# Kernel optimization log

Measured on AMD Instinct MI355X. Metric: run time of the kernel, lower is better.

## Reference

```python
import jax, jax.numpy as jnp
import numpy as np

N = 50000   # nodes
E = 800000  # edges
H = 128     # hidden dim
V = 50000   # feats_per_node (embedding vocab)


def setup_inputs() -> dict:
    key = jax.random.key(0)
    ks = jax.random.split(key, 16)
    s = 0.05  # keep activations in a sane range
    return {
        "node_ids": jax.random.randint(ks[0], (N,), 0, V),
        "src": jax.random.randint(ks[1], (E,), 0, N),
        "dst": jnp.sort(jax.random.randint(ks[2], (E,), 0, N)),
        "emb": jax.random.normal(ks[3], (V, H), jnp.float32) * s,
        "W_pool1": jax.random.normal(ks[4], (H, H), jnp.float32) * s,
        "b_pool1": jax.random.normal(ks[5], (H,), jnp.float32) * s,
        "W_self1": jax.random.normal(ks[6], (H, H), jnp.float32) * s,
        "W_neigh1": jax.random.normal(ks[7], (H, H), jnp.float32) * s,
        "b1": jax.random.normal(ks[8], (H,), jnp.float32) * s,
        "W_pool2": jax.random.normal(ks[9], (H, H), jnp.float32) * s,
        "b_pool2": jax.random.normal(ks[10], (H,), jnp.float32) * s,
        "W_self2": jax.random.normal(ks[11], (H, H), jnp.float32) * s,
        "W_neigh2": jax.random.normal(ks[12], (H, H), jnp.float32) * s,
        "b2": jax.random.normal(ks[13], (H,), jnp.float32) * s,
    }


def _sage_pool_layer(h, src, dst, W_pool, b_pool, W_self, W_neigh, b):
    # DGL SAGEConv('pool'): per-src MLP, gather over edges, segmented max per dst.
    m = jax.nn.relu(h @ W_pool + b_pool)              # [N, H]
    msgs = m[src]                                     # [E, H] gather
    agg = jax.ops.segment_max(msgs, dst, num_segments=N,
                              indices_are_sorted=True)  # [N, H]
    agg = jnp.where(jnp.isneginf(agg), 0.0, agg)      # zero-in-degree -> 0 (DGL semantics)
    return h @ W_self + agg @ W_neigh + b


def reference(node_ids, src, dst, emb,
              W_pool1, b_pool1, W_self1, W_neigh1, b1,
              W_pool2, b_pool2, W_self2, W_neigh2, b2):
    h = emb[node_ids]                                 # embedding_h on 1-hot indices
    h = _sage_pool_layer(h, src, dst, W_pool1, b_pool1, W_self1, W_neigh1, b1)
    h = _sage_pool_layer(h, src, dst, W_pool2, b_pool2, W_self2, W_neigh2, b2)
    return h
```

## Files before the change

### kernel.cpp

```cpp
#include <hip/hip_runtime.h>

#define HD 128

typedef __attribute__((ext_vector_type(8))) short short8;
typedef __attribute__((ext_vector_type(4))) float floatx4;
typedef __attribute__((ext_vector_type(2))) unsigned short ushort2v;
typedef __attribute__((ext_vector_type(4))) unsigned int uint4v;

typedef unsigned short ushort_t;
typedef unsigned int uint_t;

__device__ __forceinline__ ushort_t f2b(float f) {
    union { float f; uint_t u; } v; v.f = f;
    uint_t r = v.u + 0x7fff + ((v.u >> 16) & 1);
    return (ushort_t)(r >> 16);
}
__device__ __forceinline__ short8 cvt8(const float* __restrict__ p) {
    float4 u = *(const float4*)p, v = *(const float4*)(p + 4);
    short8 r;
    r[0] = (short)f2b(u.x); r[1] = (short)f2b(u.y); r[2] = (short)f2b(u.z); r[3] = (short)f2b(u.w);
    r[4] = (short)f2b(v.x); r[5] = (short)f2b(v.y); r[6] = (short)f2b(v.z); r[7] = (short)f2b(v.w);
    return r;
}
__device__ __forceinline__ uint_t pkmax(uint_t a, uint_t b) {
    return __builtin_bit_cast(uint_t,
        __builtin_elementwise_max(__builtin_bit_cast(ushort2v, a),
                                  __builtin_bit_cast(ushort2v, b)));
}
__device__ __forceinline__ int lbound(const int* __restrict__ dst, int E, int v) {
    int lo = 0, hi = E;
    while (lo < hi) {
        int mid = (lo + hi) >> 1;
        if (dst[mid] < v) lo = mid + 1; else hi = mid;
    }
    return lo;
}

__global__ __launch_bounds__(256) void k_prep(const int* __restrict__ dst, int E,
                                              int* __restrict__ rp, int N,
                                              int* __restrict__ srcPad,
                                              ushort_t* __restrict__ bufM,
                                              const float* W0, const float* W1,
                                              const float* W2, const float* W3,
                                              const float* W4, const float* W5,
                                              ushort_t* __restrict__ Wpk,
                                              int nbR, int nbP) {
    int b = blockIdx.x;
    if (b < nbR) {
        int i = b * 256 + threadIdx.x;
        if (i > N) return;
        rp[i] = lbound(dst, E, i);
    } else if (b < nbR + nbP) {
        int bb = b - nbR;
        const float* Ws[6] = {W0, W1, W2, W3, W4, W5};
        int mat = bb >> 6;
        int o = ((bb & 63) << 8) + threadIdx.x;
        int j = o & 7, l = (o >> 3) & 63, s = (o >> 9) & 3, t = o >> 11;
        int k = s * 32 + ((l >> 4) & 3) * 8 + j;
        int n = t * 16 + (l & 15);
        Wpk[(size_t)mat * 16384 + o] = f2b(Ws[mat][k * HD + n]);
    } else {
        int bb = b - nbR - nbP;
        if (bb == 0 && threadIdx.x < 64) {
            uint_t* mz = (uint_t*)bufM;
            mz[(size_t)(threadIdx.x >> 4) * ((size_t)(N + 1) * 16)
               + (size_t)N * 16 + (threadIdx.x & 15)] = 0u;
        }
        int idx = bb * 256 + threadIdx.x;
        if (idx < N * 32) srcPad[idx] = N;
    }
}

__device__ __forceinline__ void stage_w(const ushort_t* __restrict__ g,
                                        ushort_t* l, int tid) {
#pragma unroll
    for (int i = 0; i < 8; ++i) {
        int off = i * 2048 + tid * 8;
        *(short8*)&l[off] = *(const short8*)&g[off];
    }
}
__device__ __forceinline__ void stage_w_half(const ushort_t* __restrict__ g,
                                             ushort_t* l, int tid) {
#pragma unroll
    for (int i = 0; i < 4; ++i) {
        int off = i * 2048 + tid * 8;
        *(short8*)&l[off] = *(const short8*)&g[off];
    }
}

__device__ __forceinline__ void store_bf16(ushort_t* __restrict__ m, int row,
                                           int colbase, const floatx4& acc,
                                           const float4& bv, bool relu, int N) {
    if (row >= N) return;
    float v0 = acc[0] + bv.x, v1 = acc[1] + bv.y, v2 = acc[2] + bv.z, v3 = acc[3] + bv.w;
    if (relu) { v0 = fmaxf(v0, 0.f); v1 = fmaxf(v1, 0.f); v2 = fmaxf(v2, 0.f); v3 = fmaxf(v3, 0.f); }
    uint2 o; o.x = (uint_t)f2b(v0) | ((uint_t)f2b(v1) << 16);
    o.y = (uint_t)f2b(v2) | ((uint_t)f2b(v3) << 16);
    *(uint2*)&m[(size_t)row * HD + colbase] = o;
}

__device__ __forceinline__ void store_m(ushort_t* __restrict__ m, int row,
                                        int colbase, const floatx4& acc,
                                        const float4& bv, int N) {
    if (row >= N) return;
    float v0 = fmaxf(acc[0] + bv.x, 0.f), v1 = fmaxf(acc[1] + bv.y, 0.f);
    float v2 = fmaxf(acc[2] + bv.z, 0.f), v3 = fmaxf(acc[3] + bv.w, 0.f);
    uint2 o; o.x = (uint_t)f2b(v0) | ((uint_t)f2b(v1) << 16);
    o.y = (uint_t)f2b(v2) | ((uint_t)f2b(v3) << 16);
    size_t addr = (size_t)(colbase >> 5) * ((size_t)(N + 1) * 32)
                + (size_t)row * 32 + (colbase & 31);
    *(uint2*)&m[addr] = o;
}

__global__ __launch_bounds__(256) void k_gather_pool(const int* __restrict__ ids,
                                                     const float* __restrict__ emb,
                                                     const ushort_t* __restrict__ Wpk,
                                                     const float* __restrict__ bias,
                                                     ushort_t* __restrict__ h0,
                                                     ushort_t* __restrict__ m, int N,
                                                     const int* __restrict__ src,
                                                     const int* __restrict__ dst,
                                                     const int* __restrict__ rp,
                                                     int* __restrict__ srcPad,
                                                     int E, int nb_gemm) {
    if ((int)blockIdx.x >= nb_gemm) {
        int e = (blockIdx.x - nb_gemm) * 256 + threadIdx.x;
        if (e < E) {
            int node = dst[e];
            int j = e - rp[node];
            if (j < 32) srcPad[(size_t)node * 32 + j] = src[e];
        }
        return;
    }
    __shared__ ushort_t Wl[16384];
    int wave = blockIdx.x * 4 + (threadIdx.x >> 6);
    int row0 = wave * 32;
    int l = threadIdx.x & 63;
    int ar0 = row0 + (l & 15); if (ar0 >= N) ar0 = N - 1;
    int ar1 = ar0 + 16;        if (ar1 >= N) ar1 = N - 1;
    int ac = (l >> 4) * 8;
    int id0 = ids[ar0], id1 = ids[ar1];
    short8 a0[4], a1[4];
#pragma unroll
    for (int s = 0; s < 4; ++s) {
        a0[s] = cvt8(&emb[(size_t)id0 * HD + s * 32 + ac]);
        a1[s] = cvt8(&emb[(size_t)id1 * HD + s * 32 + ac]);
    }
    stage_w(Wpk, Wl, threadIdx.x);
    __syncthreads();
    if (row0 >= N) return;
#pragma unroll
    for (int s = 0; s < 4; ++s) {
        *(short8*)&h0[(size_t)ar0 * HD + s * 32 + ac] = a0[s];
        *(short8*)&h0[(size_t)ar1 * HD + s * 32 + ac] = a1[s];
    }
    int g0 = row0 + (l & 15), g1 = g0 + 16;
    int cb0 = ((l >> 4) & 3) * 4;
#pragma unroll
    for (int t = 0; t < 8; ++t) {
        floatx4 acc0 = {0.f, 0.f, 0.f, 0.f};
        floatx4 acc1 = {0.f, 0.f, 0.f, 0.f};
#pragma unroll
        for (int s = 0; s < 4; ++s) {
            short8 w = *(const short8*)&Wl[(t * 4 + s) * 512 + l * 8];
            acc0 = __builtin_amdgcn_mfma_f32_16x16x32_bf16(w, a0[s], acc0, 0, 0, 0);
            acc1 = __builtin_amdgcn_mfma_f32_16x16x32_bf16(w, a1[s], acc1, 0, 0, 0);
        }
        int cb = t * 16 + cb0;
        float4 bv = *(const float4*)&bias[cb];
        store_m(m, g0, cb, acc0, bv, N);
        store_m(m, g1, cb, acc1, bv, N);
    }
}

__global__ __launch_bounds__(256) void k_pool(const ushort_t* __restrict__ h,
                                              const ushort_t* __restrict__ Wpk,
                                              const float* __restrict__ bias,
                                              ushort_t* __restrict__ m, int N) {
    __shared__ ushort_t Wl[8192];
    int colhalf = blockIdx.x & 1;
    int wave = (blockIdx.x >> 1) * 4 + (threadIdx.x >> 6);
    int row0 = wave * 32;
    int l = threadIdx.x & 63;
    int ar0 = row0 + (l & 15); if (ar0 >= N) ar0 = N - 1;
    int ar1 = ar0 + 16;        if (ar1 >= N) ar1 = N - 1;
    int ac = (l >> 4) * 8;
    short8 a0[4], a1[4];
#pragma unroll
    for (int s = 0; s < 4; ++s) {
        a0[s] = *(const short8*)&h[(size_t)ar0 * HD + s * 32 + ac];
        a1[s] = *(const short8*)&h[(size_t)ar1 * HD + s * 32 + ac];
    }
    stage_w_half(Wpk + colhalf * 8192, Wl, threadIdx.x);
    __syncthreads();
    if (row0 >= N) return;
    int g0 = row0 + (l & 15), g1 = g0 + 16;
    int cb0 = ((l >> 4) & 3) * 4;
#pragma unroll
    for (int t = 0; t < 4; ++t) {
        floatx4 acc0 = {0.f, 0.f, 0.f, 0.f};
        floatx4 acc1 = {0.f, 0.f, 0.f, 0.f};
#pragma unroll
        for (int s = 0; s < 4; ++s) {
            short8 w = *(const short8*)&Wl[(t * 4 + s) * 512 + l * 8];
            acc0 = __builtin_amdgcn_mfma_f32_16x16x32_bf16(w, a0[s], acc0, 0, 0, 0);
            acc1 = __builtin_amdgcn_mfma_f32_16x16x32_bf16(w, a1[s], acc1, 0, 0, 0);
        }
        int cb = (colhalf * 4 + t) * 16 + cb0;
        float4 bv = *(const float4*)&bias[cb];
        store_m(m, g0, cb, acc0, bv, N);
        store_m(m, g1, cb, acc1, bv, N);
    }
}

__global__ __launch_bounds__(256) void k_segmax(const ushort_t* __restrict__ m,
                                                const int* __restrict__ srcPad,
                                                const int* __restrict__ src,
                                                const int* __restrict__ rp,
                                                ushort_t* __restrict__ agg, int N) {
    int cg = blockIdx.x & 3;
    int l = threadIdx.x & 63;
    int slot = l >> 2;
    int c = l & 3;
    int node0 = ((blockIdx.x >> 2) * 4 + (threadIdx.x >> 6)) * 4;
    if (node0 >= N) return;
    const uint_t* __restrict__ mg = (const uint_t*)m + (size_t)cg * ((size_t)(N + 1) * 16);
    uint_t* __restrict__ aggw = (uint_t*)agg;

    int nd[4], s0[4], s1[4], bg[4], en[4];
#pragma unroll
    for (int nn = 0; nn < 4; ++nn) {
        int node = node0 + nn; if (node >= N) node = N - 1;
        nd[nn] = node;
    }
#pragma unroll
    for (int nn = 0; nn < 4; ++nn) {
        s0[nn] = srcPad[(size_t)nd[nn] * 32 + slot];
        s1[nn] = srcPad[(size_t)nd[nn] * 32 + 16 + slot];
    }
#pragma unroll
    for (int nn = 0; nn < 4; ++nn) {
        bg[nn] = rp[nd[nn]];
        en[nn] = rp[nd[nn] + 1];
    }
    uint4v p0[4], p1[4];
#pragma unroll
    for (int nn = 0; nn < 4; ++nn) {
        p0[nn] = *(const uint4v*)&mg[(size_t)s0[nn] * 16 + c * 4];
        p1[nn] = *(const uint4v*)&mg[(size_t)s1[nn] * 16 + c * 4];
    }
    int b0 = slot & 1, b1 = (slot >> 1) & 1;
#pragma unroll
    for (int nn = 0; nn < 4; ++nn) {
        int node = node0 + nn;
        uint_t a0 = pkmax(p0[nn].x, p1[nn].x);
        uint_t a1 = pkmax(p0[nn].y, p1[nn].y);
        uint_t a2 = pkmax(p0[nn].z, p1[nn].z);
        uint_t a3 = pkmax(p0[nn].w, p1[nn].w);
        int deg = en[nn] - bg[nn];
        if (__builtin_expect(deg > 32, 0)) {
            int dm1 = deg - 1;
            for (int o = 32; o < deg; o += 16) {
                int i = o + slot; if (i > dm1) i = dm1;
                int s = src[bg[nn] + i];
                uint4v p = *(const uint4v*)&mg[(size_t)s * 16 + c * 4];
                a0 = pkmax(a0, p.x); a1 = pkmax(a1, p.y);
                a2 = pkmax(a2, p.z); a3 = pkmax(a3, p.w);
            }
        }
        uint_t q0 = b0 ? a2 : a0, q1 = b0 ? a3 : a1;
        uint_t r0 = b0 ? a0 : a2, r1 = b0 ? a1 : a3;
        q0 = pkmax(q0, (uint_t)__shfl_xor((int)r0, 4));
        q1 = pkmax(q1, (uint_t)__shfl_xor((int)r1, 4));
        uint_t s_ = b1 ? q1 : q0, t_ = b1 ? q0 : q1;
        s_ = pkmax(s_, (uint_t)__shfl_xor((int)t_, 8));
        s_ = pkmax(s_, (uint_t)__shfl_xor((int)s_, 16));
        s_ = pkmax(s_, (uint_t)__shfl_xor((int)s_, 32));
        if (slot < 4 && node < N)
            __builtin_nontemporal_store(s_,
                &aggw[(size_t)node * 64 + cg * 16 + c * 4 + 2 * b0 + b1]);
    }
}

template <bool F32OUT>
__global__ __launch_bounds__(256) void k_dual(const ushort_t* __restrict__ h,
                                              const ushort_t* __restrict__ agg,
                                              const ushort_t* __restrict__ WsPk,
                                              const ushort_t* __restrict__ WnPk,
                                              const float* __restrict__ bias,
                                              void* __restrict__ outp, int N) {
    __shared__ ushort_t Wl[16384];
    int colhalf = blockIdx.x & 1;
    int wave = (blockIdx.x >> 1) * 4 + (threadIdx.x >> 6);
    int row0 = wave * 32;
    int l = threadIdx.x & 63;
    int ar0 = row0 + (l & 15); if (ar0 >= N) ar0 = N - 1;
    int ar1 = ar0 + 16;        if (ar1 >= N) ar1 = N - 1;
    int ac = (l >> 4) * 8;
    short8 ah0[4], ah1[4], ag0[4], ag1[4];
#pragma unroll
    for (int s = 0; s < 4; ++s) {
        ah0[s] = *(const short8*)&h[(size_t)ar0 * HD + s * 32 + ac];
        ah1[s] = *(const short8*)&h[(size_t)ar1 * HD + s * 32 + ac];
        ag0[s] = *(const short8*)&agg[(size_t)ar0 * HD + s * 32 + ac];
        ag1[s] = *(const short8*)&agg[(size_t)ar1 * HD + s * 32 + ac];
    }
    stage_w_half(WsPk + colhalf * 8192, Wl, threadIdx.x);
    stage_w_half(WnPk + colhalf * 8192, Wl + 8192, threadIdx.x);
    __syncthreads();
    if (row0 >= N) return;
    int g0 = row0 + (l & 15), g1 = g0 + 16;
    int cb0 = ((l >> 4) & 3) * 4;
#pragma unroll
    for (int t = 0; t < 4; ++t) {
        floatx4 acc0 = {0.f, 0.f, 0.f, 0.f};
        floatx4 acc1 = {0.f, 0.f, 0.f, 0.f};
#pragma unroll
        for (int s = 0; s < 4; ++s) {
            short8 ws = *(const short8*)&Wl[(t * 4 + s) * 512 + l * 8];
            acc0 = __builtin_amdgcn_mfma_f32_16x16x32_bf16(ws, ah0[s], acc0, 0, 0, 0);
            acc1 = __builtin_amdgcn_mfma_f32_16x16x32_bf16(ws, ah1[s], acc1, 0, 0, 0);
        }
#pragma unroll
        for (int s = 0; s < 4; ++s) {
            short8 wn = *(const short8*)&Wl[8192 + (t * 4 + s) * 512 + l * 8];
            acc0 = __builtin_amdgcn_mfma_f32_16x16x32_bf16(wn, ag0[s], acc0, 0, 0, 0);
            acc1 = __builtin_amdgcn_mfma_f32_16x16x32_bf16(wn, ag1[s], acc1, 0, 0, 0);
        }
        int cb = (colhalf * 4 + t) * 16 + cb0;
        float4 bv = *(const float4*)&bias[cb];
        if (F32OUT) {
            float* out = (float*)outp;
            if (g0 < N) {
                float4 v = make_float4(acc0[0] + bv.x, acc0[1] + bv.y,
                                       acc0[2] + bv.z, acc0[3] + bv.w);
                *(float4*)&out[(size_t)g0 * HD + cb] = v;
            }
            if (g1 < N) {
                float4 v = make_float4(acc1[0] + bv.x, acc1[1] + bv.y,
                                       acc1[2] + bv.z, acc1[3] + bv.w);
                *(float4*)&out[(size_t)g1 * HD + cb] = v;
            }
        } else {
            ushort_t* out = (ushort_t*)outp;
            store_bf16(out, g0, cb, acc0, bv, false, N);
            store_bf16(out, g1, cb, acc1, bv, false, N);
        }
    }
}

extern "C" void kernel_launch(void* const* d_in, const int* in_sizes, int n_in,
                              void* d_out, int out_size, void* d_ws, size_t ws_size,
                              hipStream_t stream) {
    const int*   node_ids = (const int*)d_in[0];
    const int*   src      = (const int*)d_in[1];
    const int*   dst      = (const int*)d_in[2];
    const float* emb      = (const float*)d_in[3];
    const float* Wp1      = (const float*)d_in[4];
    const float* bp1      = (const float*)d_in[5];
    const float* Ws1      = (const float*)d_in[6];
    const float* Wn1      = (const float*)d_in[7];
    const float* b1       = (const float*)d_in[8];
    const float* Wp2      = (const float*)d_in[9];
    const float* bp2      = (const float*)d_in[10];
    const float* Ws2      = (const float*)d_in[11];
    const float* Wn2      = (const float*)d_in[12];
    const float* b2       = (const float*)d_in[13];
    float* out = (float*)d_out;

    const int N = in_sizes[0];
    const int E = in_sizes[1];

    char* ws = (char*)d_ws;
    int* rp = (int*)ws;
    size_t off = (((size_t)(N + 1) * 4) + 255) & ~(size_t)255;
    int* srcPad = (int*)(ws + off);
    off += (((size_t)N * 32 * 4) + 255) & ~(size_t)255;
    ushort_t* Wpk  = (ushort_t*)(ws + off);
    ushort_t* h0   = Wpk + 6 * 16384;
    ushort_t* h1   = h0 + (size_t)N * HD;
    ushort_t* bufM = h1 + (size_t)N * HD;
    ushort_t* bufA = bufM + (size_t)(N + 1) * HD;

    const int nbR = (N + 1 + 255) / 256;
    const int nbP = 6 * 64;
    const int nbI = ((N * 32) + 255) / 256;
    const int nbE = (E + 255) / 256;
    const int nb_gemm = (N + 127) / 128;
    const int nb_half = nb_gemm * 2;
    const int nb_seg  = ((N + 15) / 16) * 4;

    k_prep<<<nbR + nbP + nbI, 256, 0, stream>>>(dst, E, rp, N, srcPad, bufM,
                                                Wp1, Ws1, Wn1, Wp2, Ws2, Wn2,
                                                Wpk, nbR, nbP);

    const ushort_t* Wp1k = Wpk;
    const ushort_t* Ws1k = Wpk + 16384;
    const ushort_t* Wn1k = Wpk + 2 * 16384;
    const ushort_t* Wp2k = Wpk + 3 * 16384;
    const ushort_t* Ws2k = Wpk + 4 * 16384;
    const ushort_t* Wn2k = Wpk + 5 * 16384;

    k_gather_pool<<<nb_gemm + nbE, 256, 0, stream>>>(node_ids, emb, Wp1k, bp1,
                                                     h0, bufM, N,
                                                     src, dst, rp, srcPad, E, nb_gemm);
    k_segmax<<<nb_seg, 256, 0, stream>>>(bufM, srcPad, src, rp, bufA, N);
    k_dual<false><<<nb_half, 256, 0, stream>>>(h0, bufA, Ws1k, Wn1k, b1, h1, N);
    k_pool<<<nb_half, 256, 0, stream>>>(h1, Wp2k, bp2, bufM, N);
    k_segmax<<<nb_seg, 256, 0, stream>>>(bufM, srcPad, src, rp, bufA, N);
    k_dual<true><<<nb_half, 256, 0, stream>>>(h1, bufA, Ws2k, Wn2k, b2, out, N);
}
```

Before: 228.3 us.

## Fuse layer-1 self/neighbor GEMM with layer-2 pool GEMM in one kernel

Replaces the separate k_dual<false> and k_pool launches with a single k_dual_pool kernel. Each block computes the full 128-column h1 tile for 128 rows, writes it to global memory and also to a swizzled LDS tile, then reuses it from LDS as the A operand for the layer-2 pool GEMM. This removes one kernel launch and the global re-read of h1, and changes the grid from split column halves to full-width rows. In exchange LDS use doubles to 64KB per block, more weight staging and syncs happen per block, and the grid has half as many blocks, which may lower occupancy.

New measurement: 219.0 us. -4.1%, faster.

```diff
diff --git a/kernel.cpp b/kernel.cpp
--- a/kernel.cpp
+++ b/kernel.cpp
@@ -173,46 +173,6 @@
     }
 }
 
-__global__ __launch_bounds__(256) void k_pool(const ushort_t* __restrict__ h,
-                                              const ushort_t* __restrict__ Wpk,
-                                              const float* __restrict__ bias,
-                                              ushort_t* __restrict__ m, int N) {
-    __shared__ ushort_t Wl[8192];
-    int colhalf = blockIdx.x & 1;
-    int wave = (blockIdx.x >> 1) * 4 + (threadIdx.x >> 6);
-    int row0 = wave * 32;
-    int l = threadIdx.x & 63;
-    int ar0 = row0 + (l & 15); if (ar0 >= N) ar0 = N - 1;
-    int ar1 = ar0 + 16;        if (ar1 >= N) ar1 = N - 1;
-    int ac = (l >> 4) * 8;
-    short8 a0[4], a1[4];
-#pragma unroll
-    for (int s = 0; s < 4; ++s) {
-        a0[s] = *(const short8*)&h[(size_t)ar0 * HD + s * 32 + ac];
-        a1[s] = *(const short8*)&h[(size_t)ar1 * HD + s * 32 + ac];
-    }
-    stage_w_half(Wpk + colhalf * 8192, Wl, threadIdx.x);
-    __syncthreads();
-    if (row0 >= N) return;
-    int g0 = row0 + (l & 15), g1 = g0 + 16;
-    int cb0 = ((l >> 4) & 3) * 4;
-#pragma unroll
-    for (int t = 0; t < 4; ++t) {
-        floatx4 acc0 = {0.f, 0.f, 0.f, 0.f};
-        floatx4 acc1 = {0.f, 0.f, 0.f, 0.f};
-#pragma unroll
-        for (int s = 0; s < 4; ++s) {
-            short8 w = *(const short8*)&Wl[(t * 4 + s) * 512 + l * 8];
-            acc0 = __builtin_amdgcn_mfma_f32_16x16x32_bf16(w, a0[s], acc0, 0, 0, 0);
-            acc1 = __builtin_amdgcn_mfma_f32_16x16x32_bf16(w, a1[s], acc1, 0, 0, 0);
-        }
-        int cb = (colhalf * 4 + t) * 16 + cb0;
-        float4 bv = *(const float4*)&bias[cb];
-        store_m(m, g0, cb, acc0, bv, N);
-        store_m(m, g1, cb, acc1, bv, N);
-    }
-}
-
 __global__ __launch_bounds__(256) void k_segmax(const ushort_t* __restrict__ m,
                                                 const int* __restrict__ srcPad,
                                                 const int* __restrict__ src,
@@ -279,6 +239,104 @@
         if (slot < 4 && node < N)
             __builtin_nontemporal_store(s_,
                 &aggw[(size_t)node * 64 + cg * 16 + c * 4 + 2 * b0 + b1]);
+    }
+}
+
+__global__ __launch_bounds__(256) void k_dual_pool(const ushort_t* __restrict__ h,
+                                                   const ushort_t* __restrict__ agg,
+                                                   const ushort_t* __restrict__ WsPk,
+                                                   const ushort_t* __restrict__ WnPk,
+                                                   const ushort_t* __restrict__ WpPk,
+                                                   const float* __restrict__ bias1,
+                                                   const float* __restrict__ biasP,
+                                                   ushort_t* __restrict__ h1out,
+                                                   ushort_t* __restrict__ m2, int N) {
+    __shared__ ushort_t Wl[16384];
+    __shared__ ushort_t Ht[16384];
+    int wave = threadIdx.x >> 6;
+    int row0 = blockIdx.x * 128 + wave * 32;
+    int l = threadIdx.x & 63;
+    int ar0 = row0 + (l & 15); if (ar0 >= N) ar0 = N - 1;
+    int ar1 = ar0 + 16;        if (ar1 >= N) ar1 = N - 1;
+    int ac = (l >> 4) * 8;
+    short8 ah0[4], ah1[4], ag0[4], ag1[4];
+#pragma unroll
+    for (int s = 0; s < 4; ++s) {
+        ah0[s] = *(const short8*)&h[(size_t)ar0 * HD + s * 32 + ac];
+        ah1[s] = *(const short8*)&h[(size_t)ar1 * HD + s * 32 + ac];
+        ag0[s] = *(const short8*)&agg[(size_t)ar0 * HD + s * 32 + ac];
+        ag1[s] = *(const short8*)&agg[(size_t)ar1 * HD + s * 32 + ac];
+    }
+    int g0 = row0 + (l & 15), g1 = g0 + 16;
+    int cb0 = ((l >> 4) & 3) * 4;
+    char* ht = (char*)(Ht + wave * 4096);
+    int trow0 = l & 15, trow1 = trow0 + 16;
+    int swz0 = (trow0 & 7) << 4, swz1 = swz0;
+
+#pragma unroll
+    for (int half = 0; half < 2; ++half) {
+        if (half == 1) __syncthreads();
+        stage_w_half(WsPk + half * 8192, Wl, threadIdx.x);
+        stage_w_half(WnPk + half * 8192, Wl + 8192, threadIdx.x);
+        __syncthreads();
+#pragma unroll
+        for (int t = 0; t < 4; ++t) {
+            floatx4 acc0 = {0.f, 0.f, 0.f, 0.f};
+            floatx4 acc1 = {0.f, 0.f, 0.f, 0.f};
+#pragma unroll
+            for (int s = 0; s < 4; ++s) {
+                short8 ws = *(const short8*)&Wl[(t * 4 + s) * 512 + l * 8];
+                acc0 = __builtin_amdgcn_mfma_f32_16x16x32_bf16(ws, ah0[s], acc0, 0, 0, 0);
+                acc1 = __builtin_amdgcn_mfma_f32_16x16x32_bf16(ws, ah1[s], acc1, 0, 0, 0);
+            }
+#pragma unroll
+            for (int s = 0; s < 4; ++s) {
+                short8 wn = *(const short8*)&Wl[8192 + (t * 4 + s) * 512 + l * 8];
+                acc0 = __builtin_amdgcn_mfma_f32_16x16x32_bf16(wn, ag0[s], acc0, 0, 0, 0);
+                acc1 = __builtin_amdgcn_mfma_f32_16x16x32_bf16(wn, ag1[s], acc1, 0, 0, 0);
+            }
+            int cb = (half * 4 + t) * 16 + cb0;
+            float4 bv = *(const float4*)&bias1[cb];
+            uint2 o0, o1;
+            o0.x = (uint_t)f2b(acc0[0] + bv.x) | ((uint_t)f2b(acc0[1] + bv.y) << 16);
+            o0.y = (uint_t)f2b(acc0[2] + bv.z) | ((uint_t)f2b(acc0[3] + bv.w) << 16);
+            o1.x = (uint_t)f2b(acc1[0] + bv.x) | ((uint_t)f2b(acc1[1] + bv.y) << 16);
+            o1.y = (uint_t)f2b(acc1[2] + bv.z) | ((uint_t)f2b(acc1[3] + bv.w) << 16);
+            if (g0 < N) *(uint2*)&h1out[(size_t)g0 * HD + cb] = o0;
+            if (g1 < N) *(uint2*)&h1out[(size_t)g1 * HD + cb] = o1;
+            *(uint2*)(ht + ((trow0 * 256 + cb * 2) ^ swz0)) = o0;
+            *(uint2*)(ht + ((trow1 * 256 + cb * 2) ^ swz1)) = o1;
+        }
+    }
+
+    short8 pa0[4], pa1[4];
+#pragma unroll
+    for (int s = 0; s < 4; ++s) {
+        int colb = (s * 32 + (l >> 4) * 8) * 2;
+        pa0[s] = *(const short8*)(ht + ((trow0 * 256 + colb) ^ swz0));
+        pa1[s] = *(const short8*)(ht + ((trow1 * 256 + colb) ^ swz1));
+    }
+
+#pragma unroll
+    for (int half = 0; half < 2; ++half) {
+        __syncthreads();
+        stage_w_half(WpPk + half * 8192, Wl, threadIdx.x);
+        __syncthreads();
+#pragma unroll
+        for (int t = 0; t < 4; ++t) {
+            floatx4 acc0 = {0.f, 0.f, 0.f, 0.f};
+            floatx4 acc1 = {0.f, 0.f, 0.f, 0.f};
+#pragma unroll
+            for (int s = 0; s < 4; ++s) {
+                short8 w = *(const short8*)&Wl[(t * 4 + s) * 512 + l * 8];
+                acc0 = __builtin_amdgcn_mfma_f32_16x16x32_bf16(w, pa0[s], acc0, 0, 0, 0);
+                acc1 = __builtin_amdgcn_mfma_f32_16x16x32_bf16(w, pa1[s], acc1, 0, 0, 0);
+            }
+            int cb = (half * 4 + t) * 16 + cb0;
+            float4 bv = *(const float4*)&biasP[cb];
+            store_m(m2, g0, cb, acc0, bv, N);
+            store_m(m2, g1, cb, acc1, bv, N);
+        }
     }
 }
 
@@ -405,8 +463,8 @@
                                                      h0, bufM, N,
                                                      src, dst, rp, srcPad, E, nb_gemm);
     k_segmax<<<nb_seg, 256, 0, stream>>>(bufM, srcPad, src, rp, bufA, N);
-    k_dual<false><<<nb_half, 256, 0, stream>>>(h0, bufA, Ws1k, Wn1k, b1, h1, N);
-    k_pool<<<nb_half, 256, 0, stream>>>(h1, Wp2k, bp2, bufM, N);
+    k_dual_pool<<<nb_gemm, 256, 0, stream>>>(h0, bufA, Ws1k, Wn1k, Wp2k,
+                                             b1, bp2, h1, bufM, N);
     k_segmax<<<nb_seg, 256, 0, stream>>>(bufM, srcPad, src, rp, bufA, N);
     k_dual<true><<<nb_half, 256, 0, stream>>>(h1, bufA, Ws2k, Wn2k, b2, out, N);
 }
```
